# Kernel tuning notes

Hardware: AMD Instinct MI355X
Metric: run time of the kernel (lower is better)

The kernel has to match this reference:

```python
import math
import jax, jax.numpy as jnp
import numpy as np

B, V, E = 16, 4096, 768  # batch, vocab_size (== seq_len), embed_size


def setup_inputs() -> dict:
    key = jax.random.key(0)
    k0, k1, k2, k3, k4 = jax.random.split(key, 5)
    return {
        "sequence": jax.random.normal(k0, (B, V, 3), dtype=jnp.float32),
        # Per-vocab-index Linear(1, E): weight w[v] (shape [E]) and bias b[v] (shape [E])
        "flux_w": jax.random.normal(k1, (V, E), dtype=jnp.float32) * 0.02,
        "flux_b": jax.random.normal(k2, (V, E), dtype=jnp.float32) * 0.02,
        "time_w": jax.random.normal(k3, (V, E), dtype=jnp.float32) * 0.02,
        "time_b": jax.random.normal(k4, (V, E), dtype=jnp.float32) * 0.02,
    }


def reference(sequence, flux_w, flux_b, time_w, time_b):
    # sequence: [B, V, 3]; channel 0 -> flux, 1 -> passend (position), 2 -> time
    # FluxEmbedding: vocab_size tiny Linear(1,E) layers == per-index affine gather
    flux = sequence[..., 0:1] * flux_w + flux_b          # [B, V, E]
    time = sequence[..., 2:3] * time_w + time_b          # [B, V, E]

    # PassendEmbedding: sinusoidal encoding of the passend channel
    passend = sequence[..., 1]                           # [B, V]
    div_term = jnp.exp(
        jnp.arange(0, E, 2, dtype=jnp.float32) * (-math.log(10000.0) / E)
    )                                                    # [E/2]
    ang = passend[..., None] * div_term                  # [B, V, E/2]
    # interleave sin/cos: pe[..., 0::2]=sin, pe[..., 1::2]=cos
    pe = jnp.stack([jnp.sin(ang), jnp.cos(ang)], axis=-1).reshape(B, V, E)

    # Dropout is identity in eval mode
    return flux + pe + time
```

## Files before the change

### kernel.cpp

```cpp
#include <hip/hip_runtime.h>

#define BB 16
#define VV 4096
#define EE 768
#define E4 (EE / 4)
#define BLOCK 256
#define GRID 1536
#define SPAN (GRID * BLOCK)

typedef float f4 __attribute__((ext_vector_type(4)));

__global__ __launch_bounds__(BLOCK, 6) void bert_embed_kernel(
    const float* __restrict__ seq,
    const float* __restrict__ flux_w,
    const float* __restrict__ flux_b,
    const float* __restrict__ time_w,
    const float* __restrict__ time_b,
    float* __restrict__ out)
{
    int tid = blockIdx.x * BLOCK + threadIdx.x;
    int e4  = tid % E4;
    int v0  = tid / E4;

    const float C1     = -0.011992630692677323f;
    const float INV2PI = 0.15915494309189535f;
    float d0 = __expf((float)(4 * e4) * C1) * INV2PI;
    float d1 = __expf((float)(4 * e4 + 2) * C1) * INV2PI;

#pragma unroll 1
    for (int rep = 0; rep < 2; ++rep) {
        int v = __builtin_amdgcn_readfirstlane(v0 + rep * (SPAN / E4));

        const size_t we = (size_t)v * EE + (size_t)e4 * 4;
        f4 fw = *(const f4*)(flux_w + we);
        f4 tw = *(const f4*)(time_w + we);
        f4 fb = *(const f4*)(flux_b + we);
        f4 tb = *(const f4*)(time_b + we);
        f4 cb = fb + tb;

        const float* sp = seq + (size_t)v * 3;
        float* op = out + we;

#pragma unroll
        for (int b = 0; b < BB; ++b) {
            float s0 = sp[0];
            float s1 = sp[1];
            float s2 = sp[2];

            float r0  = s1 * d0;
            float r1  = s1 * d1;
            float sn0 = __builtin_amdgcn_sinf(r0);
            float cs0 = __builtin_amdgcn_cosf(r0);
            float sn1 = __builtin_amdgcn_sinf(r1);
            float cs1 = __builtin_amdgcn_cosf(r1);

            f4 o;
            o.x = fmaf(s0, fw.x, fmaf(s2, tw.x, cb.x)) + sn0;
            o.y = fmaf(s0, fw.y, fmaf(s2, tw.y, cb.y)) + cs0;
            o.z = fmaf(s0, fw.z, fmaf(s2, tw.z, cb.z)) + sn1;
            o.w = fmaf(s0, fw.w, fmaf(s2, tw.w, cb.w)) + cs1;
            __builtin_nontemporal_store(o, (f4*)op);

            sp += (size_t)VV * 3;
            op += (size_t)VV * EE;
        }
    }
}

extern "C" void kernel_launch(void* const* d_in, const int* in_sizes, int n_in,
                              void* d_out, int out_size, void* d_ws, size_t ws_size,
                              hipStream_t stream) {
    const float* seq = (const float*)d_in[0];
    const float* fw  = (const float*)d_in[1];
    const float* fb  = (const float*)d_in[2];
    const float* tw  = (const float*)d_in[3];
    const float* tb  = (const float*)d_in[4];
    float* out = (float*)d_out;

    bert_embed_kernel<<<GRID, BLOCK, 0, stream>>>(seq, fw, fb, tw, tb, out);
}
```

Before: 251.1 us.

## Flatten batch loop into grid-stride rows, reloading weights per output row

The kernel drops the inner batch loop that reused the four weight vectors across all 16 batch entries. It now walks a flat grid-stride loop over (batch, vocab) rows and reloads the weights and sequence values for every output row. This gives a simpler loop with fewer live registers and removes the occupancy hint, but weight reads rise by up to 16x, leaving more of the reuse to the L2 cache.

```diff
diff --git a/kernel.cpp b/kernel.cpp
--- a/kernel.cpp
+++ b/kernel.cpp
@@ -7,10 +7,12 @@
 #define BLOCK 256
 #define GRID 1536
 #define SPAN (GRID * BLOCK)
+#define TOTAL4 (BB * VV * E4)
+#define ITERS (TOTAL4 / SPAN)
 
 typedef float f4 __attribute__((ext_vector_type(4)));
 
-__global__ __launch_bounds__(BLOCK, 6) void bert_embed_kernel(
+__global__ __launch_bounds__(BLOCK) void bert_embed_kernel(
     const float* __restrict__ seq,
     const float* __restrict__ flux_w,
     const float* __restrict__ flux_b,
@@ -18,52 +20,48 @@
     const float* __restrict__ time_b,
     float* __restrict__ out)
 {
-    int tid = blockIdx.x * BLOCK + threadIdx.x;
-    int e4  = tid % E4;
-    int v0  = tid / E4;
+    const int tid  = blockIdx.x * BLOCK + threadIdx.x;
+    const int e4   = tid % E4;
+    const int row0 = tid / E4;
 
     const float C1     = -0.011992630692677323f;
     const float INV2PI = 0.15915494309189535f;
-    float d0 = __expf((float)(4 * e4) * C1) * INV2PI;
-    float d1 = __expf((float)(4 * e4 + 2) * C1) * INV2PI;
+    const float d0 = __expf((float)(4 * e4) * C1) * INV2PI;
+    const float d1 = __expf((float)(4 * e4 + 2) * C1) * INV2PI;
 
-#pragma unroll 1
-    for (int rep = 0; rep < 2; ++rep) {
-        int v = __builtin_amdgcn_readfirstlane(v0 + rep * (SPAN / E4));
+    const size_t ecol = (size_t)e4 * 4;
 
-        const size_t we = (size_t)v * EE + (size_t)e4 * 4;
+#pragma unroll 2
+    for (int it = 0; it < ITERS; ++it) {
+        int row = row0 + it * (SPAN / E4);
+        int v   = row & (VV - 1);
+        int b   = row >> 12;
+
+        const float* sp = seq + ((size_t)b * VV + v) * 3;
+        float s0 = sp[0];
+        float s1 = sp[1];
+        float s2 = sp[2];
+
+        const size_t we = (size_t)v * EE + ecol;
         f4 fw = *(const f4*)(flux_w + we);
         f4 tw = *(const f4*)(time_w + we);
         f4 fb = *(const f4*)(flux_b + we);
         f4 tb = *(const f4*)(time_b + we);
-        f4 cb = fb + tb;
 
-        const float* sp = seq + (size_t)v * 3;
-        float* op = out + we;
+        float r0  = s1 * d0;
+        float r1  = s1 * d1;
+        float sn0 = __builtin_amdgcn_sinf(r0);
+        float cs0 = __builtin_amdgcn_cosf(r0);
+        float sn1 = __builtin_amdgcn_sinf(r1);
+        float cs1 = __builtin_amdgcn_cosf(r1);
 
-#pragma unroll
-        for (int b = 0; b < BB; ++b) {
-            float s0 = sp[0];
-            float s1 = sp[1];
-            float s2 = sp[2];
+        f4 o;
+        o.x = fmaf(s0, fw.x, fmaf(s2, tw.x, fb.x + tb.x)) + sn0;
+        o.y = fmaf(s0, fw.y, fmaf(s2, tw.y, fb.y + tb.y)) + cs0;
+        o.z = fmaf(s0, fw.z, fmaf(s2, tw.z, fb.z + tb.z)) + sn1;
+        o.w = fmaf(s0, fw.w, fmaf(s2, tw.w, fb.w + tb.w)) + cs1;
 
-            float r0  = s1 * d0;
-            float r1  = s1 * d1;
-            float sn0 = __builtin_amdgcn_sinf(r0);
-            float cs0 = __builtin_amdgcn_cosf(r0);
-            float sn1 = __builtin_amdgcn_sinf(r1);
-            float cs1 = __builtin_amdgcn_cosf(r1);
-
-            f4 o;
-            o.x = fmaf(s0, fw.x, fmaf(s2, tw.x, cb.x)) + sn0;
-            o.y = fmaf(s0, fw.y, fmaf(s2, tw.y, cb.y)) + cs0;
-            o.z = fmaf(s0, fw.z, fmaf(s2, tw.z, cb.z)) + sn1;
-            o.w = fmaf(s0, fw.w, fmaf(s2, tw.w, cb.w)) + cs1;
-            __builtin_nontemporal_store(o, (f4*)op);
-
-            sp += (size_t)VV * 3;
-            op += (size_t)VV * EE;
-        }
+        __builtin_nontemporal_store(o, (f4*)(out + (size_t)row * EE + ecol));
     }
 }
 
```

Result: faster. 244.2 us (-2.8%).
